# Optimization experiments

Hardware: AMD Instinct MI355X
Metric: run time of the kernel (lower is better)

## Reference

```python
import jax, jax.numpy as jnp
import numpy as np

LN_EPS = 1e-5

def layernorm(x, w, b):
    # LayerNorm over last dim (head_dim), affine
    mu = jnp.mean(x, axis=-1, keepdims=True)
    var = jnp.mean(jnp.square(x - mu), axis=-1, keepdims=True)
    return (x - mu) * jax.lax.rsqrt(var + LN_EPS) * w + b

def setup_inputs() -> dict:
    key = jax.random.key(0)
    ks = jax.random.split(key, 6)
    B, N, C, H = 2, 2048, 1024, 16
    hd = C // H
    s = 1.0 / np.sqrt(C)
    return {
        "x": jax.random.normal(ks[0], (B, N, C), jnp.float32),
        "W_qkv": jax.random.normal(ks[1], (C, 3 * C), jnp.float32) * s,  # qkv_bias=False
        "qn_w": jnp.ones((hd,), jnp.float32),
        "qn_b": jnp.zeros((hd,), jnp.float32),
        "kn_w": jnp.ones((hd,), jnp.float32),
        "kn_b": jnp.zeros((hd,), jnp.float32),
        "W_proj": jax.random.normal(ks[2], (C, C), jnp.float32) * s,
        "b_proj": jnp.zeros((C,), jnp.float32),
    }

def reference(x, W_qkv, qn_w, qn_b, kn_w, kn_b, W_proj, b_proj):
    B, N, C = x.shape
    H = 16
    hd = C // H
    scale = hd ** -0.5
    qkv = (x @ W_qkv).reshape(B, N, 3, H, hd)
    qkv = jnp.transpose(qkv, (2, 0, 3, 1, 4))  # [3,B,H,N,hd]
    q, k, v = qkv[0], qkv[1], qkv[2]
    q = layernorm(q, qn_w, qn_b)
    k = layernorm(k, kn_w, kn_b)
    q = q * scale
    attn = jnp.einsum('bhnd,bhmd->bhnm', q, k)  # [B,H,N,N]
    attn = jax.nn.softmax(attn, axis=-1)  # attn_drop p=0 -> identity
    o = jnp.einsum('bhnm,bhmd->bhnd', attn, v)
    o = jnp.transpose(o, (0, 2, 1, 3)).reshape(B, N, C)
    return o @ W_proj + b_proj  # proj_drop p=0 -> identity
```

## Files before the change

kernel.cpp:

```cpp
#include <hip/hip_runtime.h>
#include <hip/hip_bf16.h>

#define B_  2
#define N_  2048
#define C_  1024
#define H_  16
#define HD_ 64
#define QSZ (B_*H_*N_*HD_)

typedef __attribute__((ext_vector_type(8))) short short8;
typedef __attribute__((ext_vector_type(4))) float floatx4;
typedef __attribute__((ext_vector_type(4))) unsigned short ushort4v;

__device__ __forceinline__ unsigned short f2bf(float f) {
    unsigned int u = __builtin_bit_cast(unsigned int, f);
    u += 0x7fff + ((u >> 16) & 1);
    return (unsigned short)(u >> 16);
}
__device__ __forceinline__ float bf2f(unsigned short h) {
    return __builtin_bit_cast(float, (unsigned int)h << 16);
}
__device__ __forceinline__ unsigned int pk2bf(float a, float b) {
    unsigned int ua = __builtin_bit_cast(unsigned int, a);
    unsigned int ub = __builtin_bit_cast(unsigned int, b);
    ua += 0x7fff + ((ua >> 16) & 1);
    ub += 0x7fff + ((ub >> 16) & 1);
    return __builtin_amdgcn_perm(ub, ua, 0x07060302);
}

__device__ __forceinline__ void g2l16(const void* g, void* l) {
    __builtin_amdgcn_global_load_lds(
        (const __attribute__((address_space(1))) void*)g,
        (__attribute__((address_space(3))) void*)l, 16, 0, 0);
}

__global__ __launch_bounds__(256) void pack_bf16_kernel(
    const float* __restrict__ src, unsigned short* __restrict__ dst)
{
    const int i = blockIdx.x * 256 + threadIdx.x;
    float4 v = ((const float4*)src)[i];
    ushort4 o = {f2bf(v.x), f2bf(v.y), f2bf(v.z), f2bf(v.w)};
    ((ushort4*)dst)[i] = o;
}

__global__ __launch_bounds__(256) void transpose_pack_kernel(
    const float* __restrict__ W, unsigned short* __restrict__ Wt,
    int Kd, int Nd)
{
    __shared__ unsigned short tl[32][34];
    const int r  = threadIdx.x >> 3;
    const int c4 = (threadIdx.x & 7) * 4;
    const int n0 = blockIdx.x * 32, k0 = blockIdx.y * 32;
    float4 v = *(const float4*)&W[(size_t)(k0 + r) * Nd + n0 + c4];
    tl[r][c4 + 0] = f2bf(v.x); tl[r][c4 + 1] = f2bf(v.y);
    tl[r][c4 + 2] = f2bf(v.z); tl[r][c4 + 3] = f2bf(v.w);
    __syncthreads();
    ushort4 o = {tl[c4 + 0][r], tl[c4 + 1][r], tl[c4 + 2][r], tl[c4 + 3][r]};
    *(ushort4*)&Wt[(size_t)(n0 + r) * Kd + k0 + c4] = o;
}

#define GEMM_CORE(A_, Bt_, Kd_, row0_, col0_)                                 \
    __shared__ unsigned short As[128 * 32];                                   \
    __shared__ unsigned short Bs[128 * 32];                                   \
    const int t    = threadIdx.x;                                             \
    const int lane = t & 63;                                                  \
    const int w    = t >> 6;                                                  \
    const int l15  = lane & 15;                                               \
    const int quad = lane >> 4;                                               \
    const int wm   = w >> 1, wn = w & 1;                                      \
    size_t aOff = (size_t)(row0_ + w * 16 + (lane >> 2)) * Kd_ + (lane & 3) * 8; \
    size_t bOff = (size_t)(col0_ + w * 16 + (lane >> 2)) * Kd_ + (lane & 3) * 8; \
    floatx4 acc[4][4];                                                        \
    _Pragma("unroll")                                                         \
    for (int i = 0; i < 4; ++i)                                               \
        _Pragma("unroll")                                                     \
        for (int j = 0; j < 4; ++j) acc[i][j] = floatx4{0.f, 0.f, 0.f, 0.f};  \
    for (int k0 = 0; k0 < Kd_; k0 += 32) {                                    \
        _Pragma("unroll")                                                     \
        for (int c = 0; c < 2; ++c) {                                         \
            g2l16(&A_[aOff + (size_t)c * 64 * Kd_ + k0],                      \
                  &As[(w * 16 + c * 64) * 32]);                               \
            g2l16(&Bt_[bOff + (size_t)c * 64 * Kd_ + k0],                     \
                  &Bs[(w * 16 + c * 64) * 32]);                               \
        }                                                                     \
        __syncthreads();                                                      \
        short8 af[4], bf[4];                                                  \
        _Pragma("unroll")                                                     \
        for (int i = 0; i < 4; ++i)                                           \
            af[i] = *(const short8*)&As[(wm * 64 + i * 16 + l15) * 32 + quad * 8]; \
        _Pragma("unroll")                                                     \
        for (int j = 0; j < 4; ++j)                                           \
            bf[j] = *(const short8*)&Bs[(wn * 64 + j * 16 + l15) * 32 + quad * 8]; \
        _Pragma("unroll")                                                     \
        for (int i = 0; i < 4; ++i)                                           \
            _Pragma("unroll")                                                 \
            for (int j = 0; j < 4; ++j)                                       \
                acc[i][j] = __builtin_amdgcn_mfma_f32_16x16x32_bf16(          \
                    af[i], bf[j], acc[i][j], 0, 0, 0);                        \
        __syncthreads();                                                      \
    }

__global__ __launch_bounds__(256) void gemm_qkv_kernel(
    const unsigned short* __restrict__ X,
    const unsigned short* __restrict__ Wt,
    unsigned short* __restrict__ qb, unsigned short* __restrict__ kb,
    unsigned short* __restrict__ vb)
{
    const int row0 = blockIdx.y * 128;
    const int col0 = blockIdx.x * 128;
    GEMM_CORE(X, Wt, 1024, row0, col0)
    #pragma unroll
    for (int j = 0; j < 4; ++j) {
        const int gcol = col0 + wn * 64 + j * 16 + l15;
        const int which = gcol >> 10;
        const int rem = gcol & 1023;
        const int h = rem >> 6, d = rem & 63;
        unsigned short* dstbuf = (which == 0) ? qb : (which == 1) ? kb : vb;
        #pragma unroll
        for (int i = 0; i < 4; ++i) {
            #pragma unroll
            for (int r = 0; r < 4; ++r) {
                const int grow = row0 + wm * 64 + i * 16 + quad * 4 + r;
                const int bidx = grow >> 11, n = grow & 2047;
                dstbuf[(((size_t)(bidx * H_ + h) * N_ + n) * HD_) + d] =
                    f2bf(acc[i][j][r]);
            }
        }
    }
}

__global__ __launch_bounds__(256) void gemm_proj_kernel(
    const unsigned short* __restrict__ O,
    const unsigned short* __restrict__ Wt,
    const float* __restrict__ bias, float* __restrict__ out)
{
    const int row0 = blockIdx.y * 128;
    const int col0 = blockIdx.x * 128;
    GEMM_CORE(O, Wt, 1024, row0, col0)
    #pragma unroll
    for (int j = 0; j < 4; ++j) {
        const int gcol = col0 + wn * 64 + j * 16 + l15;
        const float b = bias[gcol];
        #pragma unroll
        for (int i = 0; i < 4; ++i) {
            #pragma unroll
            for (int r = 0; r < 4; ++r) {
                const int grow = row0 + wm * 64 + i * 16 + quad * 4 + r;
                out[(size_t)grow * 1024 + gcol] = acc[i][j][r] + b;
            }
        }
    }
}

#define QSCALE 0.18033688011112042f
__global__ __launch_bounds__(256) void ln_kernel(
    unsigned short* __restrict__ qb, unsigned short* __restrict__ kb,
    const float* __restrict__ qw, const float* __restrict__ qbi,
    const float* __restrict__ kw, const float* __restrict__ kbi)
{
    const int lane = threadIdx.x & 63;
    const int w    = threadIdx.x >> 6;
    const int row  = blockIdx.x * 4 + w;
    const bool isq = (blockIdx.y == 0);
    unsigned short* p = (isq ? qb : kb) + (size_t)row * 64 + lane;
    const float* wt = isq ? qw : kw;
    const float* bi = isq ? qbi : kbi;
    float v = bf2f(*p);
    float s = v;
    #pragma unroll
    for (int o = 1; o < 64; o <<= 1) s += __shfl_xor(s, o);
    const float mu = s * (1.0f / 64.0f);
    const float d  = v - mu;
    float s2 = d * d;
    #pragma unroll
    for (int o = 1; o < 64; o <<= 1) s2 += __shfl_xor(s2, o);
    const float var = s2 * (1.0f / 64.0f);
    float y = d * rsqrtf(var + 1e-5f) * wt[lane] + bi[lane];
    if (isq) y *= QSCALE;
    *p = f2bf(y);
}

__global__ __launch_bounds__(512, 4) void flash_kernel(
    const unsigned short* __restrict__ qb, const unsigned short* __restrict__ kb,
    const unsigned short* __restrict__ vb, unsigned short* __restrict__ ob)
{
    __shared__ __align__(16) unsigned short Ks[64 * 72];
    __shared__ __align__(16) unsigned short Vt[64 * 72];
    __shared__ __align__(16) unsigned short Ps[128 * 72];
    const int t    = threadIdx.x;
    const int lane = t & 63;
    const int w    = t >> 6;
    const int l15  = lane & 15;
    const int quad = lane >> 4;
    const int q0   = blockIdx.x * 128;
    const int bh   = blockIdx.y;
    const unsigned short* Q = qb + (size_t)bh * N_ * HD_;
    const unsigned short* K = kb + (size_t)bh * N_ * HD_;
    const unsigned short* V = vb + (size_t)bh * N_ * HD_;

    {
        const int r = t >> 3, c = (t & 7) * 8;
        *(short8*)&Ps[r * 72 + c] =
            *(const short8*)&Q[(size_t)(q0 + r) * 64 + c];
        *(short8*)&Ps[(r + 64) * 72 + c] =
            *(const short8*)&Q[(size_t)(q0 + r + 64) * 64 + c];
    }
    __syncthreads();
    short8 qf[2];
    #pragma unroll
    for (int kk = 0; kk < 2; ++kk)
        qf[kk] = *(const short8*)&Ps[(w * 16 + l15) * 72 + kk * 32 + quad * 8];

    floatx4 acc[4];
    #pragma unroll
    for (int dt = 0; dt < 4; ++dt) acc[dt] = floatx4{0.f, 0.f, 0.f, 0.f};
    float m_i = -1e30f, l_i = 0.f;

    const int kvb = (t & 31) * 2;
    const int db  = (t >> 5) * 4;

    for (int kt = 0; kt < N_; kt += 64) {
        __syncthreads();
        {
            const int r = t >> 3, c = (t & 7) * 8;
            *(short8*)&Ks[r * 72 + c] =
                *(const short8*)&K[(size_t)(kt + r) * 64 + c];
            ushort4v r0 = *(const ushort4v*)&V[(size_t)(kt + kvb + 0) * 64 + db];
            ushort4v r1 = *(const ushort4v*)&V[(size_t)(kt + kvb + 1) * 64 + db];
            #pragma unroll
            for (int j = 0; j < 4; ++j) {
                unsigned int pk = (unsigned int)r0[j] | ((unsigned int)r1[j] << 16);
                *(unsigned int*)&Vt[(db + j) * 72 + kvb] = pk;
            }
        }
        __syncthreads();

        floatx4 sc[4];
        #pragma unroll
        for (int ct = 0; ct < 4; ++ct) {
            short8 a0 = *(const short8*)&Ks[(ct * 16 + l15) * 72 + quad * 8];
            short8 a1 = *(const short8*)&Ks[(ct * 16 + l15) * 72 + 32 + quad * 8];
            floatx4 r = {0.f, 0.f, 0.f, 0.f};
            r = __builtin_amdgcn_mfma_f32_16x16x32_bf16(a0, qf[0], r, 0, 0, 0);
            r = __builtin_amdgcn_mfma_f32_16x16x32_bf16(a1, qf[1], r, 0, 0, 0);
            sc[ct] = r;
        }

        {
            float mx = m_i;
            #pragma unroll
            for (int ct = 0; ct < 4; ++ct)
                #pragma unroll
                for (int r = 0; r < 4; ++r) mx = fmaxf(mx, sc[ct][r]);
            mx = fmaxf(mx, __shfl_xor(mx, 16));
            mx = fmaxf(mx, __shfl_xor(mx, 32));
            float sum = 0.f;
            #pragma unroll
            for (int ct = 0; ct < 4; ++ct)
                #pragma unroll
                for (int r = 0; r < 4; ++r) {
                    const float p = __builtin_amdgcn_exp2f(sc[ct][r] - mx);
                    sc[ct][r] = p;
                    sum += p;
                }
            sum += __shfl_xor(sum, 16);
            sum += __shfl_xor(sum, 32);
            const float alpha = __builtin_amdgcn_exp2f(m_i - mx);
            l_i = l_i * alpha + sum;
            m_i = mx;
            #pragma unroll
            for (int dt = 0; dt < 4; ++dt) acc[dt] *= alpha;
            const int prow = w * 16 + l15;
            #pragma unroll
            for (int ct = 0; ct < 4; ++ct) {
                uint2 pk;
                pk.x = pk2bf(sc[ct][0], sc[ct][1]);
                pk.y = pk2bf(sc[ct][2], sc[ct][3]);
                *(uint2*)&Ps[prow * 72 + ct * 16 + quad * 4] = pk;
            }
        }
        asm volatile("" ::: "memory");

        #pragma unroll
        for (int kk = 0; kk < 2; ++kk) {
            short8 pb = *(const short8*)
                &Ps[(w * 16 + l15) * 72 + kk * 32 + quad * 8];
            #pragma unroll
            for (int dt = 0; dt < 4; ++dt) {
                short8 va = *(const short8*)
                    &Vt[(dt * 16 + l15) * 72 + kk * 32 + quad * 8];
                acc[dt] = __builtin_amdgcn_mfma_f32_16x16x32_bf16(
                    va, pb, acc[dt], 0, 0, 0);
            }
        }
    }

    asm volatile("" ::: "memory");
    {
        const float inv = 1.0f / l_i;
        const int orow = w * 16 + l15;
        #pragma unroll
        for (int dt = 0; dt < 4; ++dt) {
            uint2 o2;
            o2.x = pk2bf(acc[dt][0] * inv, acc[dt][1] * inv);
            o2.y = pk2bf(acc[dt][2] * inv, acc[dt][3] * inv);
            *(uint2*)&Ps[orow * 72 + dt * 16 + quad * 4] = o2;
        }
    }
    __syncthreads();
    const int bidx = bh >> 4, h = bh & 15;
    {
        const int r = t >> 3, c = (t & 7) * 8;
        *(short8*)&ob[((size_t)(bidx * N_ + q0 + r)) * C_ + h * 64 + c] =
            *(const short8*)&Ps[r * 72 + c];
        *(short8*)&ob[((size_t)(bidx * N_ + q0 + r + 64)) * C_ + h * 64 + c] =
            *(const short8*)&Ps[(r + 64) * 72 + c];
    }
}

extern "C" void kernel_launch(void* const* d_in, const int* in_sizes, int n_in,
                              void* d_out, int out_size, void* d_ws, size_t ws_size,
                              hipStream_t stream) {
    const float* x      = (const float*)d_in[0];
    const float* W_qkv  = (const float*)d_in[1];
    const float* qn_w   = (const float*)d_in[2];
    const float* qn_b   = (const float*)d_in[3];
    const float* kn_w   = (const float*)d_in[4];
    const float* kn_b   = (const float*)d_in[5];
    const float* W_proj = (const float*)d_in[6];
    const float* b_proj = (const float*)d_in[7];
    float* out = (float*)d_out;

    unsigned short* qb  = (unsigned short*)d_ws;
    unsigned short* kb  = qb + (size_t)QSZ;
    unsigned short* vb  = kb + (size_t)QSZ;
    unsigned short* ob  = vb + (size_t)QSZ;
    unsigned short* xb  = ob + (size_t)B_ * N_ * C_;
    unsigned short* wqt = xb + (size_t)B_ * N_ * C_;
    unsigned short* wpt = wqt + (size_t)3 * C_ * C_;

    pack_bf16_kernel<<<dim3((B_ * N_ * C_) / 1024), 256, 0, stream>>>(x, xb);
    transpose_pack_kernel<<<dim3(96, 32), 256, 0, stream>>>(W_qkv, wqt, 1024, 3072);
    transpose_pack_kernel<<<dim3(32, 32), 256, 0, stream>>>(W_proj, wpt, 1024, 1024);
    gemm_qkv_kernel<<<dim3(24, 32), 256, 0, stream>>>(xb, wqt, qb, kb, vb);
    ln_kernel<<<dim3((B_ * H_ * N_) / 4, 2), 256, 0, stream>>>(qb, kb, qn_w, qn_b, kn_w, kn_b);
    flash_kernel<<<dim3(N_ / 128, B_ * H_), 512, 0, stream>>>(qb, kb, vb, ob);
    gemm_proj_kernel<<<dim3(8, 32), 256, 0, stream>>>(ob, wpt, b_proj, out);
}
```

Baseline: 244.2 us.

## Widen flash KV tile to 128 and prefetch next K/V tile into registers

The flash attention loop now processes 128 keys per iteration instead of 64, which halves the number of barrier pairs and online-softmax rescales. The next tile's K and V are loaded from global memory into registers right after the LDS stores, so those loads overlap with the current tile's MFMA and softmax work. In exchange the kernel uses more LDS (about 60KB versus 27KB) and more registers (score array doubled plus prefetch registers), which may reduce occupancy under the 512x4 launch bounds.

Result: faster. 226.4 us (-7.3%).

```diff
diff --git a/kernel.cpp b/kernel.cpp
--- a/kernel.cpp
+++ b/kernel.cpp
@@ -184,9 +184,9 @@
     const unsigned short* __restrict__ qb, const unsigned short* __restrict__ kb,
     const unsigned short* __restrict__ vb, unsigned short* __restrict__ ob)
 {
-    __shared__ __align__(16) unsigned short Ks[64 * 72];
-    __shared__ __align__(16) unsigned short Vt[64 * 72];
-    __shared__ __align__(16) unsigned short Ps[128 * 72];
+    __shared__ __align__(16) unsigned short Ks[128 * 72];
+    __shared__ __align__(16) unsigned short Vt[64 * 136];
+    __shared__ __align__(16) unsigned short Pb[128 * 136];
     const int t    = threadIdx.x;
     const int lane = t & 63;
     const int w    = t >> 6;
@@ -200,44 +200,52 @@
 
     {
         const int r = t >> 3, c = (t & 7) * 8;
-        *(short8*)&Ps[r * 72 + c] =
+        *(short8*)&Pb[r * 136 + c] =
             *(const short8*)&Q[(size_t)(q0 + r) * 64 + c];
-        *(short8*)&Ps[(r + 64) * 72 + c] =
+        *(short8*)&Pb[(r + 64) * 136 + c] =
             *(const short8*)&Q[(size_t)(q0 + r + 64) * 64 + c];
     }
     __syncthreads();
     short8 qf[2];
     #pragma unroll
     for (int kk = 0; kk < 2; ++kk)
-        qf[kk] = *(const short8*)&Ps[(w * 16 + l15) * 72 + kk * 32 + quad * 8];
+        qf[kk] = *(const short8*)&Pb[(w * 16 + l15) * 136 + kk * 32 + quad * 8];
 
     floatx4 acc[4];
     #pragma unroll
     for (int dt = 0; dt < 4; ++dt) acc[dt] = floatx4{0.f, 0.f, 0.f, 0.f};
     float m_i = -1e30f, l_i = 0.f;
 
-    const int kvb = (t & 31) * 2;
-    const int db  = (t >> 5) * 4;
-
-    for (int kt = 0; kt < N_; kt += 64) {
+    const int kr  = t >> 2, kc = (t & 3) * 16;
+    const int vkv = (t & 63) * 2, vd = w * 8;
+
+    short8 kA = *(const short8*)&K[(size_t)kr * 64 + kc];
+    short8 kB = *(const short8*)&K[(size_t)kr * 64 + kc + 8];
+    short8 vA = *(const short8*)&V[(size_t)vkv * 64 + vd];
+    short8 vB = *(const short8*)&V[(size_t)(vkv + 1) * 64 + vd];
+
+    for (int kt = 0; kt < N_; kt += 128) {
         __syncthreads();
-        {
-            const int r = t >> 3, c = (t & 7) * 8;
-            *(short8*)&Ks[r * 72 + c] =
-                *(const short8*)&K[(size_t)(kt + r) * 64 + c];
-            ushort4v r0 = *(const ushort4v*)&V[(size_t)(kt + kvb + 0) * 64 + db];
-            ushort4v r1 = *(const ushort4v*)&V[(size_t)(kt + kvb + 1) * 64 + db];
-            #pragma unroll
-            for (int j = 0; j < 4; ++j) {
-                unsigned int pk = (unsigned int)r0[j] | ((unsigned int)r1[j] << 16);
-                *(unsigned int*)&Vt[(db + j) * 72 + kvb] = pk;
-            }
+        *(short8*)&Ks[kr * 72 + kc]     = kA;
+        *(short8*)&Ks[kr * 72 + kc + 8] = kB;
+        #pragma unroll
+        for (int j = 0; j < 8; ++j) {
+            unsigned int pk = (unsigned int)(unsigned short)vA[j] |
+                              ((unsigned int)(unsigned short)vB[j] << 16);
+            *(unsigned int*)&Vt[(vd + j) * 136 + vkv] = pk;
         }
         __syncthreads();
-
-        floatx4 sc[4];
-        #pragma unroll
-        for (int ct = 0; ct < 4; ++ct) {
+        if (kt + 128 < N_) {
+            const int kt2 = kt + 128;
+            kA = *(const short8*)&K[(size_t)(kt2 + kr) * 64 + kc];
+            kB = *(const short8*)&K[(size_t)(kt2 + kr) * 64 + kc + 8];
+            vA = *(const short8*)&V[(size_t)(kt2 + vkv) * 64 + vd];
+            vB = *(const short8*)&V[(size_t)(kt2 + vkv + 1) * 64 + vd];
+        }
+
+        floatx4 sc[8];
+        #pragma unroll
+        for (int ct = 0; ct < 8; ++ct) {
             short8 a0 = *(const short8*)&Ks[(ct * 16 + l15) * 72 + quad * 8];
             short8 a1 = *(const short8*)&Ks[(ct * 16 + l15) * 72 + 32 + quad * 8];
             floatx4 r = {0.f, 0.f, 0.f, 0.f};
@@ -249,14 +257,14 @@
         {
             float mx = m_i;
             #pragma unroll
-            for (int ct = 0; ct < 4; ++ct)
+            for (int ct = 0; ct < 8; ++ct)
                 #pragma unroll
                 for (int r = 0; r < 4; ++r) mx = fmaxf(mx, sc[ct][r]);
             mx = fmaxf(mx, __shfl_xor(mx, 16));
             mx = fmaxf(mx, __shfl_xor(mx, 32));
             float sum = 0.f;
             #pragma unroll
-            for (int ct = 0; ct < 4; ++ct)
+            for (int ct = 0; ct < 8; ++ct)
                 #pragma unroll
                 for (int r = 0; r < 4; ++r) {
                     const float p = __builtin_amdgcn_exp2f(sc[ct][r] - mx);
@@ -272,25 +280,25 @@
             for (int dt = 0; dt < 4; ++dt) acc[dt] *= alpha;
             const int prow = w * 16 + l15;
             #pragma unroll
-            for (int ct = 0; ct < 4; ++ct) {
+            for (int ct = 0; ct < 8; ++ct) {
                 uint2 pk;
                 pk.x = pk2bf(sc[ct][0], sc[ct][1]);
                 pk.y = pk2bf(sc[ct][2], sc[ct][3]);
-                *(uint2*)&Ps[prow * 72 + ct * 16 + quad * 4] = pk;
+                *(uint2*)&Pb[prow * 136 + ct * 16 + quad * 4] = pk;
             }
         }
         asm volatile("" ::: "memory");
 
         #pragma unroll
-        for (int kk = 0; kk < 2; ++kk) {
-            short8 pb = *(const short8*)
-                &Ps[(w * 16 + l15) * 72 + kk * 32 + quad * 8];
+        for (int kk = 0; kk < 4; ++kk) {
+            short8 pbf = *(const short8*)
+                &Pb[(w * 16 + l15) * 136 + kk * 32 + quad * 8];
             #pragma unroll
             for (int dt = 0; dt < 4; ++dt) {
                 short8 va = *(const short8*)
-                    &Vt[(dt * 16 + l15) * 72 + kk * 32 + quad * 8];
+                    &Vt[(dt * 16 + l15) * 136 + kk * 32 + quad * 8];
                 acc[dt] = __builtin_amdgcn_mfma_f32_16x16x32_bf16(
-                    va, pb, acc[dt], 0, 0, 0);
+                    va, pbf, acc[dt], 0, 0, 0);
             }
         }
     }
@@ -304,7 +312,7 @@
             uint2 o2;
             o2.x = pk2bf(acc[dt][0] * inv, acc[dt][1] * inv);
             o2.y = pk2bf(acc[dt][2] * inv, acc[dt][3] * inv);
-            *(uint2*)&Ps[orow * 72 + dt * 16 + quad * 4] = o2;
+            *(uint2*)&Pb[orow * 136 + dt * 16 + quad * 4] = o2;
         }
     }
     __syncthreads();
@@ -312,9 +320,9 @@
     {
         const int r = t >> 3, c = (t & 7) * 8;
         *(short8*)&ob[((size_t)(bidx * N_ + q0 + r)) * C_ + h * 64 + c] =
-            *(const short8*)&Ps[r * 72 + c];
+            *(const short8*)&Pb[r * 136 + c];
         *(short8*)&ob[((size_t)(bidx * N_ + q0 + r + 64)) * C_ + h * 64 + c] =
-            *(const short8*)&Ps[(r + 64) * 72 + c];
+            *(const short8*)&Pb[(r + 64) * 136 + c];
     }
 }
 
```
